# Optimization experiments

Hardware: AMD Instinct MI355X
Metric: run time of the kernel (lower is better)

The kernel has to match this reference:

```python
import jax, jax.numpy as jnp
import numpy as np

N = 2048
IN_DIM = 256
OUT_DIM = 64
N_HEADS = 8  # head_dim == n_heads required by a: Linear(2*n_heads, 1)
NEG_BIG = -9.0e15


def setup_inputs() -> dict:
    key = jax.random.key(0)
    k1, k2, k3, k4 = jax.random.split(key, 4)
    h = jax.random.normal(k1, (N, IN_DIM), dtype=jnp.float32)
    adj = jax.random.randint(k2, (N, N), 0, 2, dtype=jnp.int32)
    # xavier_uniform with gain=1.414 for W: bound = gain*sqrt(6/(fan_in+fan_out))
    bw = 1.414 * np.sqrt(6.0 / (IN_DIM + OUT_DIM))
    W_w = jax.random.uniform(k3, (OUT_DIM, IN_DIM), minval=-bw, maxval=bw, dtype=jnp.float32)
    W_b = jnp.zeros((OUT_DIM,), dtype=jnp.float32)
    ba = 1.414 * np.sqrt(6.0 / (2 * N_HEADS + 1))
    a_w = jax.random.uniform(k4, (1, 2 * N_HEADS), minval=-ba, maxval=ba, dtype=jnp.float32)
    a_b = jnp.zeros((1,), dtype=jnp.float32)
    return {"h": h, "adj": adj, "W_w": W_w, "W_b": W_b, "a_w": a_w, "a_b": a_b}


def reference(h, adj, W_w, W_b, a_w, a_b):
    H = a_w.shape[1] // 2
    out_dim = W_w.shape[0]
    Dh = out_dim // H  # == H by construction
    n = h.shape[0]
    wh = h @ W_w.T + W_b                      # [N, out_dim]
    wh_head = wh.reshape(n, H, Dh)            # [N, H, Dh]
    aL = a_w[0, :Dh]                           # applies to source node i features
    aR = a_w[0, Dh:]                           # applies to node j features
    e_i = jnp.einsum('nhd,d->nh', wh_head, aL)  # [N, H]
    e_j = jnp.einsum('nhd,d->nh', wh_head, aR)  # [N, H]
    # scores[i,j,h] without materializing the N*N concat tensor
    scores = e_i[:, None, :] + e_j[None, :, :] + a_b[0]   # [N, N, H]
    scores = jnp.where(scores >= 0, scores, 0.2 * scores)  # leaky_relu(0.2)
    masked = jnp.where(adj[:, :, None] > 0, scores, NEG_BIG)
    att = jax.nn.softmax(masked, axis=1)       # normalize over j
    # out[h,i,d] = sum_j att[i,j,h] * wh_head[j,h,d]
    out = jnp.einsum('ijh,jhd->hid', att, wh_head)  # [H, N, Dh]
    out = jax.nn.elu(out)
    return out.reshape(-1, out_dim)            # faithful to .view(-1, out_dim)
```

## Files before the change

### kernel.cpp

```cpp
#include <hip/hip_runtime.h>
#include <math.h>

#define NN 2048
#define INDIM 256
#define ODIM 64
#define NH 8
#define DHD 8
#define LOG2E 1.44269504088896340736f

__global__ __launch_bounds__(256) void gat_pre(
    const float* __restrict__ h, const float* __restrict__ Ww,
    const float* __restrict__ Wb, const float* __restrict__ aw,
    const float* __restrict__ ab,
    float* __restrict__ wh, float* __restrict__ eiL, float* __restrict__ ejL)
{
    __shared__ float sH[16][INDIM];
    const int t = threadIdx.x;
    const int n0 = blockIdx.x * 16;
    {
        const float4* src = (const float4*)(h + (size_t)n0 * INDIM);
        float4* dst = (float4*)&sH[0][0];
#pragma unroll
        for (int k = 0; k < 4; ++k) dst[t + k * 256] = src[t + k * 256];
    }
    __syncthreads();

    const int o  = t & 63;
    const int wv = t >> 6;
    const int nb = wv * 4;
    const float4* w4 = (const float4*)(Ww + (size_t)o * INDIM);
    float a0 = 0.f, a1 = 0.f, a2 = 0.f, a3 = 0.f;
#pragma unroll 4
    for (int k = 0; k < INDIM / 4; ++k) {
        const float4 wk = w4[k];
        const float4 h0 = *(const float4*)&sH[nb + 0][k * 4];
        const float4 h1 = *(const float4*)&sH[nb + 1][k * 4];
        const float4 h2 = *(const float4*)&sH[nb + 2][k * 4];
        const float4 h3 = *(const float4*)&sH[nb + 3][k * 4];
        a0 = fmaf(wk.x, h0.x, a0); a0 = fmaf(wk.y, h0.y, a0);
        a0 = fmaf(wk.z, h0.z, a0); a0 = fmaf(wk.w, h0.w, a0);
        a1 = fmaf(wk.x, h1.x, a1); a1 = fmaf(wk.y, h1.y, a1);
        a1 = fmaf(wk.z, h1.z, a1); a1 = fmaf(wk.w, h1.w, a1);
        a2 = fmaf(wk.x, h2.x, a2); a2 = fmaf(wk.y, h2.y, a2);
        a2 = fmaf(wk.z, h2.z, a2); a2 = fmaf(wk.w, h2.w, a2);
        a3 = fmaf(wk.x, h3.x, a3); a3 = fmaf(wk.y, h3.y, a3);
        a3 = fmaf(wk.z, h3.z, a3); a3 = fmaf(wk.w, h3.w, a3);
    }
    const float bias = Wb[o];
    float accs[4] = {a0 + bias, a1 + bias, a2 + bias, a3 + bias};

    const int d = o & 7;
    const float aL = aw[d], aR = aw[NH + d];
    const float abv = ab[0];
#pragma unroll
    for (int r = 0; r < 4; ++r) {
        const int n = n0 + nb + r;
        wh[(size_t)n * ODIM + o] = accs[r];
        float pi = accs[r] * aL;
        float pj = accs[r] * aR;
        pi += __shfl_xor(pi, 1, 64); pj += __shfl_xor(pj, 1, 64);
        pi += __shfl_xor(pi, 2, 64); pj += __shfl_xor(pj, 2, 64);
        pi += __shfl_xor(pi, 4, 64); pj += __shfl_xor(pj, 4, 64);
        if (d == 0) {
            const int hd = o >> 3;
            eiL[n * NH + hd] = (pi + abv) * LOG2E;
            ejL[n * NH + hd] = pj * LOG2E;
        }
    }
}

__global__ __launch_bounds__(512, 2) void gat_main(
    const int* __restrict__ adj, const float* __restrict__ wh,
    const float* __restrict__ eiL, const float* __restrict__ ejL,
    float* __restrict__ out)
{
    __shared__ float s_adj[8 * NN];
    __shared__ float s_red[8][8][8][9];
    const int t  = threadIdx.x;
    const int i0 = blockIdx.x * 8;

    {
        const int4* arow = (const int4*)(adj + (size_t)i0 * NN);
        float4* sa = (float4*)s_adj;
#pragma unroll
        for (int k = 0; k < 8; ++k) {
            const int4 v = arow[t + k * 512];
            sa[t + k * 512] = make_float4((float)v.x, (float)v.y, (float)v.z, (float)v.w);
        }
    }
    __syncthreads();

    const int hh = t & 7;
    const int jj = t >> 3;
    float eih[8];
#pragma unroll
    for (int i = 0; i < 8; ++i) eih[i] = eiL[(i0 + i) * NH + hh];

    float den[8];
    float acc[8][8];
#pragma unroll
    for (int i = 0; i < 8; ++i) {
        den[i] = 0.f;
#pragma unroll
        for (int d2 = 0; d2 < 8; ++d2) acc[i][d2] = 0.f;
    }

#pragma unroll 2
    for (int it = 0; it < NN / 64; ++it) {
        const int j = (it << 6) | jj;
        const float ejv = ejL[j * NH + hh];
        const float4* wr = (const float4*)(wh + (size_t)j * ODIM + hh * DHD);
        const float4 w0 = wr[0];
        const float4 w1 = wr[1];
#pragma unroll
        for (int i = 0; i < 8; ++i) {
            float s = eih[i] + ejv;
            s = fmaxf(s, 0.2f * s);
            float w = exp2f(s) * s_adj[i * NN + j];
            den[i] += w;
            acc[i][0] = fmaf(w, w0.x, acc[i][0]);
            acc[i][1] = fmaf(w, w0.y, acc[i][1]);
            acc[i][2] = fmaf(w, w0.z, acc[i][2]);
            acc[i][3] = fmaf(w, w0.w, acc[i][3]);
            acc[i][4] = fmaf(w, w1.x, acc[i][4]);
            acc[i][5] = fmaf(w, w1.y, acc[i][5]);
            acc[i][6] = fmaf(w, w1.z, acc[i][6]);
            acc[i][7] = fmaf(w, w1.w, acc[i][7]);
        }
    }

#pragma unroll
    for (int m = 8; m <= 32; m <<= 1) {
#pragma unroll
        for (int i = 0; i < 8; ++i) {
            den[i] += __shfl_xor(den[i], m, 64);
#pragma unroll
            for (int d2 = 0; d2 < 8; ++d2)
                acc[i][d2] += __shfl_xor(acc[i][d2], m, 64);
        }
    }
    const int lane = t & 63;
    const int wv   = t >> 6;
    if (lane < 8) {
#pragma unroll
        for (int i = 0; i < 8; ++i) {
#pragma unroll
            for (int d2 = 0; d2 < 8; ++d2) s_red[wv][lane][i][d2] = acc[i][d2];
            s_red[wv][lane][i][8] = den[i];
        }
    }
    __syncthreads();

    {
        const int i  = t >> 6;
        const int oh = (t >> 3) & 7;
        const int d2 = t & 7;
        float v = 0.f, dn = 0.f;
#pragma unroll
        for (int w2 = 0; w2 < 8; ++w2) {
            v  += s_red[w2][oh][i][d2];
            dn += s_red[w2][oh][i][8];
        }
        float r = v / dn;
        r = (r > 0.f) ? r : expm1f(r);
        out[(size_t)oh * (NN * DHD) + (size_t)(i0 + i) * DHD + d2] = r;
    }
}

extern "C" void kernel_launch(void* const* d_in, const int* in_sizes, int n_in,
                              void* d_out, int out_size, void* d_ws, size_t ws_size,
                              hipStream_t stream) {
    const float* h   = (const float*)d_in[0];
    const int*   adj = (const int*)d_in[1];
    const float* Ww  = (const float*)d_in[2];
    const float* Wb  = (const float*)d_in[3];
    const float* aw  = (const float*)d_in[4];
    const float* ab  = (const float*)d_in[5];
    float* out = (float*)d_out;

    float* wh  = (float*)d_ws;
    float* eiL = wh + (size_t)NN * ODIM;
    float* ejL = eiL + (size_t)NN * NH;

    gat_pre<<<NN / 16, 256, 0, stream>>>(h, Ww, Wb, aw, ab, wh, eiL, ejL);
    gat_main<<<NN / 8, 512, 0, stream>>>(adj, wh, eiL, ejL, out);
}
```

Measured before the change: 40.60 us.

## Split attention over j chunks, bf16 features, bitmask adjacency, add finalize kernel

The main kernel now splits the neighbor dimension into four chunks and handles four rows per block, raising the block count and occupancy. A third kernel then combines the partial numerators and denominators and applies ELU. Node features are stored as bf16 to halve their load traffic, and adjacency is packed into per-column bitmasks in shared memory instead of float rows. Masked entries use a select to a large negative exponent instead of a multiply. The changes add a kernel launch and a partial-sum round trip through global memory, and bf16 rounding of features lowers precision.

```diff
diff --git a/kernel.cpp b/kernel.cpp
--- a/kernel.cpp
+++ b/kernel.cpp
@@ -7,164 +7,175 @@
 #define NH 8
 #define DHD 8
 #define LOG2E 1.44269504088896340736f
+#define JSPLIT 4
+#define JCHUNK (NN / JSPLIT)
+#define IBLK 4
 
 __global__ __launch_bounds__(256) void gat_pre(
     const float* __restrict__ h, const float* __restrict__ Ww,
     const float* __restrict__ Wb, const float* __restrict__ aw,
     const float* __restrict__ ab,
-    float* __restrict__ wh, float* __restrict__ eiL, float* __restrict__ ejL)
+    unsigned short* __restrict__ whb, float* __restrict__ eiL,
+    float* __restrict__ ejL)
 {
-    __shared__ float sH[16][INDIM];
+    __shared__ float sH[IBLK][INDIM];
     const int t = threadIdx.x;
-    const int n0 = blockIdx.x * 16;
-    {
-        const float4* src = (const float4*)(h + (size_t)n0 * INDIM);
-        float4* dst = (float4*)&sH[0][0];
-#pragma unroll
-        for (int k = 0; k < 4; ++k) dst[t + k * 256] = src[t + k * 256];
-    }
+    const int n0 = blockIdx.x * 4;
+    ((float4*)&sH[0][0])[t] = ((const float4*)(h + (size_t)n0 * INDIM))[t];
     __syncthreads();
 
     const int o  = t & 63;
     const int wv = t >> 6;
-    const int nb = wv * 4;
+    const int n  = n0 + wv;
     const float4* w4 = (const float4*)(Ww + (size_t)o * INDIM);
-    float a0 = 0.f, a1 = 0.f, a2 = 0.f, a3 = 0.f;
-#pragma unroll 4
+    float acc = 0.f;
+#pragma unroll 8
     for (int k = 0; k < INDIM / 4; ++k) {
         const float4 wk = w4[k];
-        const float4 h0 = *(const float4*)&sH[nb + 0][k * 4];
-        const float4 h1 = *(const float4*)&sH[nb + 1][k * 4];
-        const float4 h2 = *(const float4*)&sH[nb + 2][k * 4];
-        const float4 h3 = *(const float4*)&sH[nb + 3][k * 4];
-        a0 = fmaf(wk.x, h0.x, a0); a0 = fmaf(wk.y, h0.y, a0);
-        a0 = fmaf(wk.z, h0.z, a0); a0 = fmaf(wk.w, h0.w, a0);
-        a1 = fmaf(wk.x, h1.x, a1); a1 = fmaf(wk.y, h1.y, a1);
-        a1 = fmaf(wk.z, h1.z, a1); a1 = fmaf(wk.w, h1.w, a1);
-        a2 = fmaf(wk.x, h2.x, a2); a2 = fmaf(wk.y, h2.y, a2);
-        a2 = fmaf(wk.z, h2.z, a2); a2 = fmaf(wk.w, h2.w, a2);
-        a3 = fmaf(wk.x, h3.x, a3); a3 = fmaf(wk.y, h3.y, a3);
-        a3 = fmaf(wk.z, h3.z, a3); a3 = fmaf(wk.w, h3.w, a3);
-    }
-    const float bias = Wb[o];
-    float accs[4] = {a0 + bias, a1 + bias, a2 + bias, a3 + bias};
+        const float4 hv = *(const float4*)&sH[wv][k * 4];
+        acc = fmaf(wk.x, hv.x, acc); acc = fmaf(wk.y, hv.y, acc);
+        acc = fmaf(wk.z, hv.z, acc); acc = fmaf(wk.w, hv.w, acc);
+    }
+    acc += Wb[o];
+
+    {
+        unsigned int u = __float_as_uint(acc);
+        unsigned int r = (u + 0x7FFF + ((u >> 16) & 1)) >> 16;
+        whb[(size_t)n * ODIM + o] = (unsigned short)r;
+    }
 
     const int d = o & 7;
-    const float aL = aw[d], aR = aw[NH + d];
-    const float abv = ab[0];
-#pragma unroll
-    for (int r = 0; r < 4; ++r) {
-        const int n = n0 + nb + r;
-        wh[(size_t)n * ODIM + o] = accs[r];
-        float pi = accs[r] * aL;
-        float pj = accs[r] * aR;
-        pi += __shfl_xor(pi, 1, 64); pj += __shfl_xor(pj, 1, 64);
-        pi += __shfl_xor(pi, 2, 64); pj += __shfl_xor(pj, 2, 64);
-        pi += __shfl_xor(pi, 4, 64); pj += __shfl_xor(pj, 4, 64);
-        if (d == 0) {
-            const int hd = o >> 3;
-            eiL[n * NH + hd] = (pi + abv) * LOG2E;
-            ejL[n * NH + hd] = pj * LOG2E;
-        }
-    }
-}
-
-__global__ __launch_bounds__(512, 2) void gat_main(
-    const int* __restrict__ adj, const float* __restrict__ wh,
+    float pi = acc * aw[d];
+    float pj = acc * aw[NH + d];
+    pi += __shfl_xor(pi, 1, 64); pj += __shfl_xor(pj, 1, 64);
+    pi += __shfl_xor(pi, 2, 64); pj += __shfl_xor(pj, 2, 64);
+    pi += __shfl_xor(pi, 4, 64); pj += __shfl_xor(pj, 4, 64);
+    if (d == 0) {
+        const int hd = o >> 3;
+        eiL[n * NH + hd] = (pi + ab[0]) * LOG2E;
+        ejL[n * NH + hd] = pj * LOG2E;
+    }
+}
+
+__global__ __launch_bounds__(512, 8) void gat_main(
+    const int* __restrict__ adj, const unsigned short* __restrict__ whb,
     const float* __restrict__ eiL, const float* __restrict__ ejL,
-    float* __restrict__ out)
+    float* __restrict__ pacc, float* __restrict__ pden)
 {
-    __shared__ float s_adj[8 * NN];
-    __shared__ float s_red[8][8][8][9];
+    __shared__ unsigned char s_bits[JCHUNK];
+    __shared__ float s_red[8][8][IBLK][9];
     const int t  = threadIdx.x;
-    const int i0 = blockIdx.x * 8;
+    const int i0 = (blockIdx.x >> 2) * IBLK;
+    const int js = blockIdx.x & 3;
+    const int jbase = js * JCHUNK;
 
     {
-        const int4* arow = (const int4*)(adj + (size_t)i0 * NN);
-        float4* sa = (float4*)s_adj;
-#pragma unroll
-        for (int k = 0; k < 8; ++k) {
-            const int4 v = arow[t + k * 512];
-            sa[t + k * 512] = make_float4((float)v.x, (float)v.y, (float)v.z, (float)v.w);
-        }
+        unsigned int b = 0;
+#pragma unroll
+        for (int i = 0; i < IBLK; ++i)
+            b |= (adj[(size_t)(i0 + i) * NN + jbase + t] != 0) << i;
+        s_bits[t] = (unsigned char)b;
     }
     __syncthreads();
 
     const int hh = t & 7;
     const int jj = t >> 3;
-    float eih[8];
-#pragma unroll
-    for (int i = 0; i < 8; ++i) eih[i] = eiL[(i0 + i) * NH + hh];
-
-    float den[8];
-    float acc[8][8];
-#pragma unroll
-    for (int i = 0; i < 8; ++i) {
-        den[i] = 0.f;
-#pragma unroll
-        for (int d2 = 0; d2 < 8; ++d2) acc[i][d2] = 0.f;
-    }
+    float eih[IBLK];
+#pragma unroll
+    for (int i = 0; i < IBLK; ++i) eih[i] = eiL[(i0 + i) * NH + hh];
+
+    float den[IBLK] = {0.f, 0.f, 0.f, 0.f};
+    float acc[IBLK][DHD];
+#pragma unroll
+    for (int i = 0; i < IBLK; ++i)
+#pragma unroll
+        for (int d = 0; d < DHD; ++d) acc[i][d] = 0.f;
 
 #pragma unroll 2
-    for (int it = 0; it < NN / 64; ++it) {
-        const int j = (it << 6) | jj;
+    for (int it = 0; it < JCHUNK / 64; ++it) {
+        const int jl = it * 64 + jj;
+        const int j  = jbase + jl;
         const float ejv = ejL[j * NH + hh];
-        const float4* wr = (const float4*)(wh + (size_t)j * ODIM + hh * DHD);
-        const float4 w0 = wr[0];
-        const float4 w1 = wr[1];
-#pragma unroll
-        for (int i = 0; i < 8; ++i) {
+        const uint4 wd = ((const uint4*)whb)[j * NH + hh];
+        const int bits = s_bits[jl];
+
+        float e[IBLK];
+#pragma unroll
+        for (int i = 0; i < IBLK; ++i) {
             float s = eih[i] + ejv;
             s = fmaxf(s, 0.2f * s);
-            float w = exp2f(s) * s_adj[i * NN + j];
-            den[i] += w;
-            acc[i][0] = fmaf(w, w0.x, acc[i][0]);
-            acc[i][1] = fmaf(w, w0.y, acc[i][1]);
-            acc[i][2] = fmaf(w, w0.z, acc[i][2]);
-            acc[i][3] = fmaf(w, w0.w, acc[i][3]);
-            acc[i][4] = fmaf(w, w1.x, acc[i][4]);
-            acc[i][5] = fmaf(w, w1.y, acc[i][5]);
-            acc[i][6] = fmaf(w, w1.z, acc[i][6]);
-            acc[i][7] = fmaf(w, w1.w, acc[i][7]);
+            s = (bits & (1 << i)) ? s : -192.0f;
+            e[i] = __builtin_amdgcn_exp2f(s);
+            den[i] += e[i];
+        }
+#pragma unroll
+        for (int q = 0; q < 4; ++q) {
+            const unsigned int w = (&wd.x)[q];
+            const float lo = __uint_as_float(w << 16);
+            const float hi = __uint_as_float(w & 0xFFFF0000u);
+#pragma unroll
+            for (int i = 0; i < IBLK; ++i) {
+                acc[i][2 * q]     = fmaf(e[i], lo, acc[i][2 * q]);
+                acc[i][2 * q + 1] = fmaf(e[i], hi, acc[i][2 * q + 1]);
+            }
         }
     }
 
 #pragma unroll
     for (int m = 8; m <= 32; m <<= 1) {
 #pragma unroll
-        for (int i = 0; i < 8; ++i) {
+        for (int i = 0; i < IBLK; ++i) {
             den[i] += __shfl_xor(den[i], m, 64);
 #pragma unroll
-            for (int d2 = 0; d2 < 8; ++d2)
-                acc[i][d2] += __shfl_xor(acc[i][d2], m, 64);
+            for (int d = 0; d < DHD; ++d)
+                acc[i][d] += __shfl_xor(acc[i][d], m, 64);
         }
     }
     const int lane = t & 63;
     const int wv   = t >> 6;
     if (lane < 8) {
 #pragma unroll
-        for (int i = 0; i < 8; ++i) {
-#pragma unroll
-            for (int d2 = 0; d2 < 8; ++d2) s_red[wv][lane][i][d2] = acc[i][d2];
+        for (int i = 0; i < IBLK; ++i) {
+#pragma unroll
+            for (int d = 0; d < DHD; ++d) s_red[wv][lane][i][d] = acc[i][d];
             s_red[wv][lane][i][8] = den[i];
         }
     }
     __syncthreads();
 
     {
-        const int i  = t >> 6;
-        const int oh = (t >> 3) & 7;
-        const int d2 = t & 7;
-        float v = 0.f, dn = 0.f;
-#pragma unroll
-        for (int w2 = 0; w2 < 8; ++w2) {
-            v  += s_red[w2][oh][i][d2];
-            dn += s_red[w2][oh][i][8];
-        }
-        float r = v / dn;
-        r = (r > 0.f) ? r : expm1f(r);
-        out[(size_t)oh * (NN * DHD) + (size_t)(i0 + i) * DHD + d2] = r;
-    }
+        const int i  = (t >> 7) & 3;
+        const int hD = (t >> 4) & 7;
+        const int sl = t & 15;
+        if (sl < 9) {
+            float v = 0.f;
+#pragma unroll
+            for (int w2 = 0; w2 < 8; ++w2) v += s_red[w2][hD][i][sl];
+            if (sl < 8)
+                pacc[(((size_t)js * NN + i0 + i) * NH + hD) * DHD + sl] = v;
+            else
+                pden[((size_t)js * NN + i0 + i) * NH + hD] = v;
+        }
+    }
+}
+
+__global__ __launch_bounds__(256) void gat_fin(
+    const float* __restrict__ pacc, const float* __restrict__ pden,
+    float* __restrict__ out)
+{
+    const int gid = blockIdx.x * 256 + threadIdx.x;
+    const int d = gid & 7;
+    const int hD = (gid >> 3) & 7;
+    const int i = gid >> 6;
+    float v = 0.f, dn = 0.f;
+#pragma unroll
+    for (int js = 0; js < JSPLIT; ++js) {
+        v  += pacc[(((size_t)js * NN + i) * NH + hD) * DHD + d];
+        dn += pden[((size_t)js * NN + i) * NH + hD];
+    }
+    float r = v / dn;
+    r = (r > 0.f) ? r : expm1f(r);
+    out[(size_t)hD * (NN * DHD) + (size_t)i * DHD + d] = r;
 }
 
 extern "C" void kernel_launch(void* const* d_in, const int* in_sizes, int n_in,
@@ -178,10 +189,14 @@
     const float* ab  = (const float*)d_in[5];
     float* out = (float*)d_out;
 
-    float* wh  = (float*)d_ws;
-    float* eiL = wh + (size_t)NN * ODIM;
-    float* ejL = eiL + (size_t)NN * NH;
-
-    gat_pre<<<NN / 16, 256, 0, stream>>>(h, Ww, Wb, aw, ab, wh, eiL, ejL);
-    gat_main<<<NN / 8, 512, 0, stream>>>(adj, wh, eiL, ejL, out);
-}
+    char* ws = (char*)d_ws;
+    unsigned short* whb = (unsigned short*)ws;
+    float* eiL  = (float*)(ws + 262144);
+    float* ejL  = (float*)(ws + 327680);
+    float* pacc = (float*)(ws + 393216);
+    float* pden = (float*)(ws + 2490368);
+
+    gat_pre<<<NN / 4, 256, 0, stream>>>(h, Ww, Wb, aw, ab, whb, eiL, ejL);
+    gat_main<<<(NN / IBLK) * JSPLIT, 512, 0, stream>>>(adj, whb, eiL, ejL, pacc, pden);
+    gat_fin<<<NN * ODIM / 256, 256, 0, stream>>>(pacc, pden, out);
+}
```

Result: slower. 57.17 us (+40.8%).
